# Kernel optimization log

Hardware: AMD Instinct MI355X
Metric: run time of the kernel (lower is better)

Reference implementation:

```python
import jax, jax.numpy as jnp
import numpy as np

B, D, H, K = 16384, 128, 1024, 8
OPD = 3 * K + 1  # params per dim
TB = 3.0         # tail_bound: left=bottom=-TB, right=top=TB
EPS = 1e-12
MIN_W = MIN_H = MIN_D = 1e-3


def _masks():
    rng = np.random.RandomState(0)
    in_deg = np.arange(1, D + 1)
    h1 = rng.randint(1, D, size=(H,))
    h2 = rng.randint(1, D, size=(H,))
    out_deg = np.arange(1, D + 1)
    m1 = (in_deg[None, :] <= h1[:, None]).astype(np.float32)          # [H, D]
    m2 = (h1[None, :] <= h2[:, None]).astype(np.float32)              # [H, H]
    m3 = np.repeat((out_deg[:, None] > h2[None, :]).astype(np.float32), OPD, axis=0)  # [D*OPD, H]
    return jnp.asarray(m1), jnp.asarray(m2), jnp.asarray(m3)


def _kaiming(key, fan_out, fan_in, a=0.1):
    bound = np.sqrt(6.0 / ((1.0 + a * a) * fan_in))
    return jax.random.uniform(key, (fan_out, fan_in), jnp.float32, -bound, bound)


def setup_inputs() -> dict:
    key = jax.random.key(0)
    kx, k1, k2, k3 = jax.random.split(key, 4)
    m1, m2, m3 = _masks()
    return {
        'x': jax.random.normal(kx, (B, D), jnp.float32),
        'W1': _kaiming(k1, H, D), 'b1': jnp.zeros((H,), jnp.float32),
        'W2': _kaiming(k2, H, H), 'b2': jnp.zeros((H,), jnp.float32),
        'W3': _kaiming(k3, D * OPD, H), 'b3': jnp.zeros((D * OPD,), jnp.float32),
        'm1': m1, 'm2': m2, 'm3': m3,
    }


def _norm_cum(u, mn):
    k = u.shape[-1]
    w = jax.nn.softmax(u, axis=-1)
    w = mn + (1.0 - mn * k) * w
    c = jnp.cumsum(w, axis=-1)
    c = jnp.pad(c, [(0, 0)] * (c.ndim - 1) + [(1, 0)])
    c = c / jnp.clip(c[..., -1:], 1e-12)
    return c[..., 1:] - c[..., :-1], c


def _take(p, idx):
    return jnp.take_along_axis(p, idx[..., None], axis=-1)[..., 0]


def _forward(x, W1, b1, W2, b2, W3, b3, m1, m2, m3):
    h = jax.nn.silu(x @ (W1 * m1).T + b1)
    h = jax.nn.silu(h @ (W2 * m2).T + b2)
    raw = (h @ (W3 * m3).T + b3).reshape(-1, D, OPD)  # [B, D, 3K+1]
    uw, uh, ud = raw[..., :K], raw[..., K:2 * K], raw[..., 2 * K:]
    w, cw = _norm_cum(uw, MIN_W)
    hh, ch = _norm_cum(uh, MIN_H)
    d = MIN_D + jax.nn.softplus(ud)  # [B, D, K+1]

    left, right, bottom, top = -TB, TB, -TB, TB
    inside = (x >= left) & (x <= right)  # [B, D]
    xs = jnp.clip((x - left) / (right - left), 0.0, 1.0)
    bid = jnp.clip(jnp.sum((xs[..., None] >= cw), axis=-1) - 1, 0, K - 1)
    xk, wk = _take(cw, bid), _take(w, bid)
    yk, hk = _take(ch, bid), _take(hh, bid)
    dk, dk1 = _take(d, bid), _take(d, bid + 1)
    t = jnp.clip((xs - xk) / (wk + EPS), 0.0, 1.0)
    a = (hk + EPS) / (wk + EPS)
    num = a * t * t + dk * t * (1 - t)
    den = a + (dk + dk1 - 2 * a) * t * (1 - t)
    s = num / (den + EPS)
    y = (yk + hk * s) * (top - bottom) + bottom
    dnum = a * a * (dk1 * t * t + 2 * a * t * (1 - t) + dk * (1 - t) * (1 - t))
    dydx = (top - bottom) / (right - left) * dnum / (den * den + EPS)
    out = jnp.where(inside, y, x)
    lad = jnp.where(inside, jnp.log(jnp.clip(dydx, 1e-12)), 0.0)
    return out, jnp.sum(lad, axis=-1)


def reference(x, W1, b1, W2, b2, W3, b3, m1, m2, m3):
    return _forward(x, W1, b1, W2, b2, W3, b3, m1, m2, m3)
```

## Files before the change

### kernel.cpp

```cpp
#include <hip/hip_runtime.h>
#include <hip/hip_bf16.h>

#define BATCH 16384
#define DIM   128
#define HID   1024
#define NK    8
#define OPD   25
#define N3    (DIM*OPD)
#define NP    3328

typedef __attribute__((ext_vector_type(8))) short  short8;
typedef __attribute__((ext_vector_type(4))) float  floatx4;
typedef unsigned int u32;

__device__ __forceinline__ float fexp(float x) { return __expf(x); }
__device__ __forceinline__ float flog(float x) { return __logf(x); }
__device__ __forceinline__ float fdiv(float a, float b) { return __fdividef(a, b); }

__device__ __forceinline__ void async_copy16(const unsigned short* g,
                                             unsigned short* l) {
    __builtin_amdgcn_global_load_lds(
        (const __attribute__((address_space(1))) u32*)g,
        (__attribute__((address_space(3))) u32*)l,
        16, 0, 0);
}

__device__ __forceinline__ void swizzle_bid(int bid, int NT,
                                            int& tile, int& m) {
    const int xcd  = bid & 7;
    const int u    = bid >> 3;
    const int ph   = NT * 8;
    const int half = u / ph;
    const int rem  = u % ph;
    const int trank = rem >> 3;
    const int msub  = rem & 7;
    tile = NT - 1 - trank;
    m    = xcd * 16 + half * 8 + msub;
}

__global__ __launch_bounds__(128) void hsum_kernel(
    const float* __restrict__ m1, const float* __restrict__ m3,
    int* __restrict__ h1i, int* __restrict__ h2i) {
    const int b = blockIdx.x, t = threadIdx.x;
    if (b < HID) {
        float v = m1[b * DIM + t];
        #pragma unroll
        for (int off = 32; off > 0; off >>= 1) v += __shfl_down(v, off, 64);
        __shared__ float ws[2];
        if ((t & 63) == 0) ws[t >> 6] = v;
        __syncthreads();
        if (t == 0) h1i[b] = (int)(ws[0] + ws[1] + 0.5f);
    } else {
        const int j = (b - HID) * 128 + t;
        float s = 0.f;
        for (int d = 0; d < DIM; d++) s += m3[(size_t)d * OPD * HID + j];
        h2i[j] = DIM - (int)(s + 0.5f);
    }
}

__global__ __launch_bounds__(1024) void sort_kernel(
    const int* __restrict__ h1i, const int* __restrict__ h2i,
    int* __restrict__ perm1, int* __restrict__ perm2,
    int* __restrict__ h1sv, int* __restrict__ h2sv,
    int* __restrict__ klim1, int* __restrict__ klim2, int* __restrict__ klim3)
{
    __shared__ int hist[128];
    __shared__ int h1s[1024], h2s[1024];
    const int t = threadIdx.x;
    const int h1v = h1i[t], h2v = h2i[t];

    if (t < 128) hist[t] = 0;
    __syncthreads();
    atomicAdd(&hist[h1v], 1);
    __syncthreads();
    if (t == 0) { int a = 0; for (int b = 0; b < 128; b++) { int c = hist[b]; hist[b] = a; a += c; } }
    __syncthreads();
    int r = atomicAdd(&hist[h1v], 1);
    perm1[r] = t; h1s[r] = h1v; h1sv[r] = h1v;
    __syncthreads();
    if (t < 128) hist[t] = 0;
    __syncthreads();
    atomicAdd(&hist[h2v], 1);
    __syncthreads();
    if (t == 0) { int a = 0; for (int b = 0; b < 128; b++) { int c = hist[b]; hist[b] = a; a += c; } }
    __syncthreads();
    r = atomicAdd(&hist[h2v], 1);
    perm2[r] = t; h2s[r] = h2v; h2sv[r] = h2v;
    __syncthreads();

    if (t < 8) {
        klim1[t] = ((h1s[t * 128 + 127] + 63) >> 6) << 6;
        int mh = h2s[t * 128 + 127];
        int c = 0;
        for (int j = 0; j < 1024; j++) c += (h1s[j] <= mh) ? 1 : 0;
        klim2[t] = ((c + 63) >> 6) << 6;
    }
    if (t < 26) {
        int dmax = t * 5 + 4; if (dmax > 127) dmax = 127;
        int c = 0;
        for (int j = 0; j < 1024; j++) c += (h2s[j] <= dmax) ? 1 : 0;
        klim3[t] = ((c + 63) >> 6) << 6;
    }
}

__global__ __launch_bounds__(256) void wperm_kernel(
    const float* __restrict__ W1, const float* __restrict__ b1,
    const float* __restrict__ W2, const float* __restrict__ b2,
    const float* __restrict__ W3, const float* __restrict__ x,
    const int* __restrict__ perm1, const int* __restrict__ perm2,
    const int* __restrict__ h1sv, const int* __restrict__ h2sv,
    __hip_bfloat16* __restrict__ w1p, float* __restrict__ b1p,
    __hip_bfloat16* __restrict__ w2p, float* __restrict__ b2p,
    __hip_bfloat16* __restrict__ w3p,
    __hip_bfloat16* __restrict__ xb, float* __restrict__ lad)
{
    __shared__ float row[HID];
    const int b = blockIdx.x, t = threadIdx.x;
    if (b < 512) {
        const int i = b * 256 + t;
        const int hp = i >> 7, col = i & 127;
        const int src = perm1[hp];
        float v = (col < h1sv[hp]) ? W1[src * DIM + col] : 0.f;
        w1p[i] = __float2bfloat16(v);
        if (col == 0) b1p[hp] = b1[src];
    } else if (b < 512 + HID) {
        const int ip = b - 512;
        const int si = perm2[ip];
        const int h2v = h2sv[ip];
        #pragma unroll
        for (int q = 0; q < 4; q++) row[q * 256 + t] = W2[(size_t)si * HID + q * 256 + t];
        __syncthreads();
        #pragma unroll
        for (int q = 0; q < 4; q++) {
            const int jp = q * 256 + t;
            float v = (h1sv[jp] <= h2v) ? row[perm1[jp]] : 0.f;
            w2p[(size_t)ip * HID + jp] = __float2bfloat16(v);
        }
        if (t == 0) b2p[ip] = b2[si];
    } else if (b < 512 + HID + NP) {
        const int c = b - 512 - HID;
        const int s = c & 127, t3 = c >> 7;
        if (s >= 125) {
            #pragma unroll
            for (int q = 0; q < 4; q++)
                w3p[(size_t)c * HID + q * 256 + t] = __float2bfloat16(0.f);
            return;
        }
        const int srcrow = t3 * 125 + s;
        const int d = srcrow / 25;
        #pragma unroll
        for (int q = 0; q < 4; q++) row[q * 256 + t] = W3[(size_t)srcrow * HID + q * 256 + t];
        __syncthreads();
        #pragma unroll
        for (int q = 0; q < 4; q++) {
            const int kk = q * 256 + t;
            float v = (h2sv[kk] <= d) ? row[perm2[kk]] : 0.f;
            w3p[(size_t)c * HID + kk] = __float2bfloat16(v);
        }
    } else {
        const int i = (b - (512 + HID + NP)) * 256 + t;
        xb[i] = __float2bfloat16(x[i]);
        if (i < BATCH) lad[i] = 0.f;
    }
}

__device__ __forceinline__ void spline_eval(const float* __restrict__ p,
                                            float xv, float& yout, float& lout) {
    float cw[NK + 1], ch[NK + 1];
    {
        float mx = p[0];
        #pragma unroll
        for (int j = 1; j < NK; j++) mx = fmaxf(mx, p[j]);
        float e[NK], s = 0.f;
        #pragma unroll
        for (int j = 0; j < NK; j++) { e[j] = fexp(p[j] - mx); s += e[j]; }
        const float inv = fdiv(1.f, s);
        cw[0] = 0.f;
        #pragma unroll
        for (int j = 0; j < NK; j++) cw[j + 1] = cw[j] + (0.001f + 0.992f * e[j] * inv);
    }
    {
        float mx = p[8];
        #pragma unroll
        for (int j = 1; j < NK; j++) mx = fmaxf(mx, p[8 + j]);
        float e[NK], s = 0.f;
        #pragma unroll
        for (int j = 0; j < NK; j++) { e[j] = fexp(p[8 + j] - mx); s += e[j]; }
        const float inv = fdiv(1.f, s);
        ch[0] = 0.f;
        #pragma unroll
        for (int j = 0; j < NK; j++) ch[j + 1] = ch[j] + (0.001f + 0.992f * e[j] * inv);
    }

    const bool inside = (xv >= -3.f) && (xv <= 3.f);
    float xs = (xv + 3.f) * (1.f / 6.f);
    xs = fminf(fmaxf(xs, 0.f), 1.f);
    const float xsc = xs * cw[NK];

    float xk = 0.f, wk = cw[1], yk = 0.f, hk = ch[1];
    float uda = p[16], udb = p[17];
    #pragma unroll
    for (int j = 1; j < NK; j++) {
        const bool c = (xsc >= cw[j]);
        xk  = c ? cw[j] : xk;
        wk  = c ? (cw[j + 1] - cw[j]) : wk;
        yk  = c ? ch[j] : yk;
        hk  = c ? (ch[j + 1] - ch[j]) : hk;
        uda = c ? p[16 + j] : uda;
        udb = c ? p[17 + j] : udb;
    }

    const float dk  = 0.001f + ((uda > 20.f) ? uda : flog(1.f + fexp(uda)));
    const float dk1 = 0.001f + ((udb > 20.f) ? udb : flog(1.f + fexp(udb)));

    float t = fdiv(xs - xk, wk + 1e-12f);
    t = fminf(fmaxf(t, 0.f), 1.f);
    const float a   = fdiv(hk + 1e-12f, wk + 1e-12f);
    const float omt = 1.f - t;
    const float tt1 = t * omt;
    const float num = a * t * t + dk * tt1;
    const float den = a + (dk + dk1 - 2.f * a) * tt1;
    const float s   = fdiv(num, den + 1e-12f);
    const float y   = (yk + hk * s) * 6.f - 3.f;
    const float dnum = a * a * (dk1 * t * t + 2.f * a * tt1 + dk * omt * omt);
    const float dydx = fdiv(dnum, den * den + 1e-12f);

    yout = inside ? y : xv;
    lout = inside ? flog(fmaxf(dydx, 1e-12f)) : 0.f;
}

__global__ __launch_bounds__(256, 4) void gemm_bt_kernel(
    const unsigned short* __restrict__ A,
    const unsigned short* __restrict__ Bw,
    const float* __restrict__ bias,
    const int* __restrict__ klim,
    __hip_bfloat16* __restrict__ Cout,
    int M, int N, int Kd)
{
    constexpr int BM = 128, BN = 128, BK = 64;
    __shared__ __align__(16) char smem[32768];
    unsigned short* As = (unsigned short*)smem;
    unsigned short* Bs = (unsigned short*)(smem + 16384);
    float* eb = (float*)smem;

    const int bid = blockIdx.y * gridDim.x + blockIdx.x;
    int tile, mpan;
    swizzle_bid(bid, gridDim.x, tile, mpan);
    const int bn = tile * BN;
    const int bm = mpan * BM;
    const int Klim = klim[tile];

    const int t    = threadIdx.x;
    const int lane = t & 63;
    const int w    = t >> 6;
    const int wr   = (w >> 1) * 64;
    const int wc   = (w & 1) * 64;
    const int lr   = lane & 15;
    const int quad = lane >> 4;
    const int lxor = lr & 7;

    floatx4 acc[4][4] = {};

    const int lrow = lane >> 3;
    const int lcol = ((lane & 7) ^ lrow) * 8;

    for (int k0 = 0; k0 < Klim; k0 += BK) {
        __syncthreads();
        #pragma unroll
        for (int p = 0; p < 4; p++) {
            const int q = w * 4 + p;
            const int r = q * 8 + lrow;
            async_copy16(&A[(size_t)(bm + r) * Kd + k0 + lcol],
                         &As[q * 512 + lane * 8]);
            async_copy16(&Bw[(size_t)(bn + r) * Kd + k0 + lcol],
                         &Bs[q * 512 + lane * 8]);
        }
        __syncthreads();
        #pragma unroll
        for (int ks = 0; ks < BK; ks += 32) {
            const int cbase = (ks >> 3) + quad;
            const int coff  = (cbase ^ lxor) * 8;
            short8 af[4], bfr[4];
            #pragma unroll
            for (int i = 0; i < 4; i++)
                af[i] = *(const short8*)&As[(wr + i * 16 + lr) * BK + coff];
            #pragma unroll
            for (int j = 0; j < 4; j++)
                bfr[j] = *(const short8*)&Bs[(wc + j * 16 + lr) * BK + coff];
            #pragma unroll
            for (int i = 0; i < 4; i++)
                #pragma unroll
                for (int j = 0; j < 4; j++)
                    acc[i][j] = __builtin_amdgcn_mfma_f32_16x16x32_bf16(
                        af[i], bfr[j], acc[i][j], 0, 0, 0);
        }
    }

    #pragma unroll 1
    for (int h = 0; h < 2; h++) {
        __syncthreads();
        if ((w >> 1) == h) {
            #pragma unroll
            for (int j = 0; j < 4; j++) {
                const int s = wc + j * 16 + lr;
                const float bv = bias[bn + s];
                #pragma unroll
                for (int i = 0; i < 4; i++) {
                    const int lrw = i * 16 + quad * 4;
                    #pragma unroll
                    for (int r2 = 0; r2 < 4; r2++)
                        eb[(lrw + r2) * 128 + s] = acc[i][j][r2] + bv;
                }
            }
        }
        __syncthreads();
        #pragma unroll
        for (int it = 0; it < 4; it++) {
            const int idx = it * 256 + t;
            const int row = idx >> 4;
            const int c0  = (idx & 15) << 3;
            const floatx4 v0 = *(const floatx4*)&eb[row * 128 + c0];
            const floatx4 v1 = *(const floatx4*)&eb[row * 128 + c0 + 4];
            short8 o;
            #pragma unroll
            for (int e = 0; e < 4; e++) {
                float a0 = v0[e];
                a0 = a0 * fdiv(1.f, 1.f + fexp(-a0));
                union { __hip_bfloat16 b; unsigned short u; } c0v;
                c0v.b = __float2bfloat16(a0);
                o[e] = (short)c0v.u;
                float a1 = v1[e];
                a1 = a1 * fdiv(1.f, 1.f + fexp(-a1));
                union { __hip_bfloat16 b; unsigned short u; } c1v;
                c1v.b = __float2bfloat16(a1);
                o[e + 4] = (short)c1v.u;
            }
            *(short8*)&Cout[(size_t)(bm + h * 64 + row) * N + bn + c0] = o;
        }
    }
}

__global__ __launch_bounds__(256, 4) void gemm3_spline_kernel(
    const unsigned short* __restrict__ A,
    const unsigned short* __restrict__ Bw,
    const float* __restrict__ b3,
    const int* __restrict__ klim,
    const float* __restrict__ x,
    float* __restrict__ out,
    float* __restrict__ lad,
    int M)
{
    constexpr int BM = 128, BN = 128, BK = 64, Kd = HID;
    constexpr int GS = 28;
    constexpr int RS = 140;
    __shared__ __align__(16) char smem[64 * RS * 4 + 128 * 4];
    unsigned short* As = (unsigned short*)smem;
    unsigned short* Bs = (unsigned short*)(smem + BM * BK * 2);
    float* eb     = (float*)smem;
    float* ladacc = (float*)(smem + 64 * RS * 4);

    const int bid = blockIdx.y * gridDim.x + blockIdx.x;
    int tile, mpan;
    swizzle_bid(bid, gridDim.x, tile, mpan);
    const int bn = tile * BN;
    const int bm = mpan * BM;
    const int Klim = klim[tile];

    const int t    = threadIdx.x;
    const int lane = t & 63;
    const int w    = t >> 6;
    const int wr   = (w >> 1) * 64;
    const int wc   = (w & 1) * 64;
    const int lr   = lane & 15;
    const int quad = lane >> 4;
    const int lxor = lr & 7;

    if (t < 128) ladacc[t] = 0.f;

    floatx4 acc[4][4] = {};

    const int lrow = lane >> 3;
    const int lcol = ((lane & 7) ^ lrow) * 8;

    for (int k0 = 0; k0 < Klim; k0 += BK) {
        __syncthreads();
        #pragma unroll
        for (int p = 0; p < 4; p++) {
            const int q = w * 4 + p;
            const int r = q * 8 + lrow;
            async_copy16(&A[(size_t)(bm + r) * Kd + k0 + lcol],
                         &As[q * 512 + lane * 8]);
            async_copy16(&Bw[(size_t)(bn + r) * Kd + k0 + lcol],
                         &Bs[q * 512 + lane * 8]);
        }
        __syncthreads();
        #pragma unroll
        for (int ks = 0; ks < BK; ks += 32) {
            const int cbase = (ks >> 3) + quad;
            const int coff  = (cbase ^ lxor) * 8;
            short8 af[4], bfr[4];
            #pragma unroll
            for (int i = 0; i < 4; i++)
                af[i] = *(const short8*)&As[(wr + i * 16 + lr) * BK + coff];
            #pragma unroll
            for (int j = 0; j < 4; j++)
                bfr[j] = *(const short8*)&Bs[(wc + j * 16 + lr) * BK + coff];
            #pragma unroll
            for (int i = 0; i < 4; i++)
                #pragma unroll
                for (int j = 0; j < 4; j++)
                    acc[i][j] = __builtin_amdgcn_mfma_f32_16x16x32_bf16(
                        af[i], bfr[j], acc[i][j], 0, 0, 0);
        }
    }

    #pragma unroll 1
    for (int h = 0; h < 2; h++) {
        __syncthreads();
        if ((w >> 1) == h) {
            #pragma unroll
            for (int j = 0; j < 4; j++) {
                const int s = wc + j * 16 + lr;
                if (s < 125) {
                    const int grp = s / 25, within = s % 25;
                    const int off = grp * GS + within;
                    const int bidx = tile * 125 + s;
                    const float bv = b3[bidx < N3 ? bidx : 0];
                    #pragma unroll
                    for (int i = 0; i < 4; i++) {
                        const int lrw = i * 16 + quad * 4;
                        #pragma unroll
                        for (int r2 = 0; r2 < 4; r2++)
                            eb[(lrw + r2) * RS + off] = acc[i][j][r2] + bv;
                    }
                }
            }
        }
        __syncthreads();
        #pragma unroll 1
        for (int q = t; q < 320; q += 256) {
            const int r  = q / 5;
            const int ds = q % 5;
            const int dim = tile * 5 + ds;
            if (dim < DIM) {
                float pl[28];
                const floatx4* pv = (const floatx4*)(eb + r * RS + ds * GS);
                #pragma unroll
                for (int ii = 0; ii < 7; ii++) ((floatx4*)pl)[ii] = pv[ii];
                const int grow = bm + h * 64 + r;
                const float xv = x[(size_t)grow * DIM + dim];
                float y, l;
                spline_eval(pl, xv, y, l);
                out[(size_t)grow * DIM + dim] = y;
                atomicAdd(&ladacc[h * 64 + r], l);
            }
        }
    }
    __syncthreads();
    if (t < 128) atomicAdd(&lad[bm + t], ladacc[t]);
}

extern "C" void kernel_launch(void* const* d_in, const int* in_sizes, int n_in,
                              void* d_out, int out_size, void* d_ws, size_t ws_size,
                              hipStream_t stream) {
    const float* x  = (const float*)d_in[0];
    const float* W1 = (const float*)d_in[1];
    const float* b1 = (const float*)d_in[2];
    const float* W2 = (const float*)d_in[3];
    const float* b2 = (const float*)d_in[4];
    const float* W3 = (const float*)d_in[5];
    const float* b3 = (const float*)d_in[6];
    const float* m1 = (const float*)d_in[7];
    const float* m3 = (const float*)d_in[9];

    char* ws = (char*)d_ws;
    const size_t OFF_W1B = 0;
    const size_t OFF_W2B = OFF_W1B + (size_t)HID * DIM * 2;
    const size_t OFF_W3P = OFF_W2B + (size_t)HID * HID * 2;
    const size_t OFF_XB  = OFF_W3P + (size_t)NP * HID * 2;
    const size_t OFF_H1B = OFF_XB  + (size_t)BATCH * DIM * 2;
    const size_t OFF_H2B = OFF_H1B + (size_t)BATCH * HID * 2;
    const size_t OFF_SML = OFF_H2B + (size_t)BATCH * HID * 2;

    __hip_bfloat16* w1p = (__hip_bfloat16*)(ws + OFF_W1B);
    __hip_bfloat16* w2p = (__hip_bfloat16*)(ws + OFF_W2B);
    __hip_bfloat16* w3p = (__hip_bfloat16*)(ws + OFF_W3P);
    __hip_bfloat16* xb  = (__hip_bfloat16*)(ws + OFF_XB);
    __hip_bfloat16* h1b = (__hip_bfloat16*)(ws + OFF_H1B);
    __hip_bfloat16* h2b = (__hip_bfloat16*)(ws + OFF_H2B);

    float* b1p   = (float*)(ws + OFF_SML);
    float* b2p   = b1p + HID;
    int*   h1i   = (int*)(b2p + HID);
    int*   h2i   = h1i + HID;
    int*   perm1 = h2i + HID;
    int*   perm2 = perm1 + HID;
    int*   h1sv  = perm2 + HID;
    int*   h2sv  = h1sv + HID;
    int*   klim1 = h2sv + HID;
    int*   klim2 = klim1 + 8;
    int*   klim3 = klim2 + 8;

    float* out_p = (float*)d_out;
    float* lad_p = out_p + (size_t)BATCH * DIM;

    hsum_kernel<<<HID + 8, 128, 0, stream>>>(m1, m3, h1i, h2i);
    sort_kernel<<<1, 1024, 0, stream>>>(h1i, h2i, perm1, perm2, h1sv, h2sv,
                                        klim1, klim2, klim3);
    wperm_kernel<<<512 + HID + NP + (BATCH * DIM) / 256, 256, 0, stream>>>(
        W1, b1, W2, b2, W3, x, perm1, perm2, h1sv, h2sv,
        w1p, b1p, w2p, b2p, w3p, xb, lad_p);

    gemm_bt_kernel<<<dim3(HID / 128, BATCH / 128), 256, 0, stream>>>(
        (const unsigned short*)xb, (const unsigned short*)w1p, b1p, klim1, h1b,
        BATCH, HID, DIM);
    gemm_bt_kernel<<<dim3(HID / 128, BATCH / 128), 256, 0, stream>>>(
        (const unsigned short*)h1b, (const unsigned short*)w2p, b2p, klim2, h2b,
        BATCH, HID, HID);
    gemm3_spline_kernel<<<dim3(NP / 128, BATCH / 128), 256, 0, stream>>>(
        (const unsigned short*)h2b, (const unsigned short*)w3p, b3, klim3, x,
        out_p, lad_p, BATCH);
}
```

Baseline: 263.8 us.

## Widen GEMM3 spline tile to two N-tiles per block for A reuse

The final GEMM+spline kernel now computes a 128x256 output tile per block: each block loads the A panel once and multiplies it against two adjacent 128-column weight tiles, keeping two accumulator sets. The spline epilogue runs twice, once per sub-tile, using the same LDS staging. This halves the A-panel loads and grid size, at the cost of doubled accumulator registers (possible occupancy loss under launch_bounds 256,4), a larger LDS buffer, and the K loop running to the max of the two tiles' masked K limits.

After: 365.6 us. +38.6%, slower.

```diff
diff --git a/kernel.cpp b/kernel.cpp
--- a/kernel.cpp
+++ b/kernel.cpp
@@ -350,21 +350,22 @@
     float* __restrict__ lad,
     int M)
 {
-    constexpr int BM = 128, BN = 128, BK = 64, Kd = HID;
+    constexpr int BM = 128, BK = 64, Kd = HID;
     constexpr int GS = 28;
     constexpr int RS = 140;
-    __shared__ __align__(16) char smem[64 * RS * 4 + 128 * 4];
+    __shared__ __align__(16) char smem[49152];
     unsigned short* As = (unsigned short*)smem;
-    unsigned short* Bs = (unsigned short*)(smem + BM * BK * 2);
+    unsigned short* Bs = (unsigned short*)(smem + 16384);
     float* eb     = (float*)smem;
     float* ladacc = (float*)(smem + 64 * RS * 4);
 
     const int bid = blockIdx.y * gridDim.x + blockIdx.x;
-    int tile, mpan;
-    swizzle_bid(bid, gridDim.x, tile, mpan);
-    const int bn = tile * BN;
-    const int bm = mpan * BM;
-    const int Klim = klim[tile];
+    int pair, mpan;
+    swizzle_bid(bid, gridDim.x, pair, mpan);
+    const int bn2 = pair * 256;
+    const int bm  = mpan * BM;
+    const int k0a = klim[2 * pair], k0b = klim[2 * pair + 1];
+    const int Klim = (k0a > k0b) ? k0a : k0b;
 
     const int t    = threadIdx.x;
     const int lane = t & 63;
@@ -375,9 +376,8 @@
     const int quad = lane >> 4;
     const int lxor = lr & 7;
 
-    if (t < 128) ladacc[t] = 0.f;
-
-    floatx4 acc[4][4] = {};
+    floatx4 acc0[4][4] = {};
+    floatx4 acc1[4][4] = {};
 
     const int lrow = lane >> 3;
     const int lcol = ((lane & 7) ^ lrow) * 8;
@@ -390,7 +390,12 @@
             const int r = q * 8 + lrow;
             async_copy16(&A[(size_t)(bm + r) * Kd + k0 + lcol],
                          &As[q * 512 + lane * 8]);
-            async_copy16(&Bw[(size_t)(bn + r) * Kd + k0 + lcol],
+        }
+        #pragma unroll
+        for (int p = 0; p < 8; p++) {
+            const int q = w * 8 + p;
+            const int r = q * 8 + lrow;
+            async_copy16(&Bw[(size_t)(bn2 + r) * Kd + k0 + lcol],
                          &Bs[q * 512 + lane * 8]);
         }
         __syncthreads();
@@ -409,53 +414,73 @@
             for (int i = 0; i < 4; i++)
                 #pragma unroll
                 for (int j = 0; j < 4; j++)
-                    acc[i][j] = __builtin_amdgcn_mfma_f32_16x16x32_bf16(
-                        af[i], bfr[j], acc[i][j], 0, 0, 0);
-        }
-    }
-
-    #pragma unroll 1
-    for (int h = 0; h < 2; h++) {
-        __syncthreads();
-        if ((w >> 1) == h) {
-            #pragma unroll
-            for (int j = 0; j < 4; j++) {
-                const int s = wc + j * 16 + lr;
-                if (s < 125) {
-                    const int grp = s / 25, within = s % 25;
-                    const int off = grp * GS + within;
-                    const int bidx = tile * 125 + s;
-                    const float bv = b3[bidx < N3 ? bidx : 0];
-                    #pragma unroll
-                    for (int i = 0; i < 4; i++) {
-                        const int lrw = i * 16 + quad * 4;
-                        #pragma unroll
-                        for (int r2 = 0; r2 < 4; r2++)
-                            eb[(lrw + r2) * RS + off] = acc[i][j][r2] + bv;
-                    }
-                }
-            }
-        }
-        __syncthreads();
-        #pragma unroll 1
-        for (int q = t; q < 320; q += 256) {
-            const int r  = q / 5;
-            const int ds = q % 5;
-            const int dim = tile * 5 + ds;
-            if (dim < DIM) {
-                float pl[28];
-                const floatx4* pv = (const floatx4*)(eb + r * RS + ds * GS);
+                    acc0[i][j] = __builtin_amdgcn_mfma_f32_16x16x32_bf16(
+                        af[i], bfr[j], acc0[i][j], 0, 0, 0);
+            #pragma unroll
+            for (int j = 0; j < 4; j++)
+                bfr[j] = *(const short8*)&Bs[(128 + wc + j * 16 + lr) * BK + coff];
+            #pragma unroll
+            for (int i = 0; i < 4; i++)
                 #pragma unroll
-                for (int ii = 0; ii < 7; ii++) ((floatx4*)pl)[ii] = pv[ii];
-                const int grow = bm + h * 64 + r;
-                const float xv = x[(size_t)grow * DIM + dim];
-                float y, l;
-                spline_eval(pl, xv, y, l);
-                out[(size_t)grow * DIM + dim] = y;
-                atomicAdd(&ladacc[h * 64 + r], l);
-            }
-        }
-    }
+                for (int j = 0; j < 4; j++)
+                    acc1[i][j] = __builtin_amdgcn_mfma_f32_16x16x32_bf16(
+                        af[i], bfr[j], acc1[i][j], 0, 0, 0);
+        }
+    }
+
+#define EPIPASS(ACC_, TH_)                                                     \
+    {                                                                          \
+        const int tile = pair * 2 + TH_;                                       \
+        _Pragma("unroll 1")                                                    \
+        for (int h = 0; h < 2; h++) {                                          \
+            __syncthreads();                                                   \
+            if (TH_ == 0 && h == 0 && t < 128) ladacc[t] = 0.f;                \
+            if ((w >> 1) == h) {                                               \
+                _Pragma("unroll")                                              \
+                for (int j = 0; j < 4; j++) {                                  \
+                    const int s = wc + j * 16 + lr;                            \
+                    if (s < 125) {                                             \
+                        const int grp = s / 25, within = s % 25;               \
+                        const int off = grp * GS + within;                     \
+                        const int bidx = tile * 125 + s;                       \
+                        const float bv = b3[bidx < N3 ? bidx : 0];             \
+                        _Pragma("unroll")                                      \
+                        for (int i = 0; i < 4; i++) {                          \
+                            const int lrw = i * 16 + quad * 4;                 \
+                            _Pragma("unroll")                                  \
+                            for (int r2 = 0; r2 < 4; r2++)                     \
+                                eb[(lrw + r2) * RS + off] =                    \
+                                    ACC_[i][j][r2] + bv;                       \
+                        }                                                      \
+                    }                                                          \
+                }                                                              \
+            }                                                                  \
+            __syncthreads();                                                   \
+            _Pragma("unroll 1")                                                \
+            for (int q = t; q < 320; q += 256) {                               \
+                const int r  = q / 5;                                          \
+                const int ds = q % 5;                                          \
+                const int dim = tile * 5 + ds;                                 \
+                if (dim < DIM) {                                               \
+                    float pl[28];                                              \
+                    const floatx4* pv = (const floatx4*)(eb + r * RS + ds * GS);\
+                    _Pragma("unroll")                                          \
+                    for (int ii = 0; ii < 7; ii++) ((floatx4*)pl)[ii] = pv[ii];\
+                    const int grow = bm + h * 64 + r;                          \
+                    const float xv = x[(size_t)grow * DIM + dim];              \
+                    float y, l;                                                \
+                    spline_eval(pl, xv, y, l);                                 \
+                    out[(size_t)grow * DIM + dim] = y;                         \
+                    atomicAdd(&ladacc[h * 64 + r], l);                         \
+                }                                                              \
+            }                                                                  \
+        }                                                                      \
+    }
+
+    EPIPASS(acc0, 0)
+    EPIPASS(acc1, 1)
+#undef EPIPASS
+
     __syncthreads();
     if (t < 128) atomicAdd(&lad[bm + t], ladacc[t]);
 }
@@ -517,7 +542,7 @@
     gemm_bt_kernel<<<dim3(HID / 128, BATCH / 128), 256, 0, stream>>>(
         (const unsigned short*)h1b, (const unsigned short*)w2p, b2p, klim2, h2b,
         BATCH, HID, HID);
-    gemm3_spline_kernel<<<dim3(NP / 128, BATCH / 128), 256, 0, stream>>>(
+    gemm3_spline_kernel<<<dim3(13, BATCH / 128), 256, 0, stream>>>(
         (const unsigned short*)h2b, (const unsigned short*)w3p, b3, klim3, x,
         out_p, lad_p, BATCH);
 }
```
